# Kernel optimization log

Measured on AMD Instinct MI355X. Metric: run time of the kernel, lower is better.

## Reference

```python
import jax, jax.numpy as jnp
import numpy as np

N_NODES = 50000
N_EDGES = 800000
D_FEAT = 128
N_LAYERS = 3
HALF = 64  # units // 2 per kernel in tf_geometric MeanGraphSage
HIDDEN = 256
NUM_LABELS = 40


def setup_inputs() -> dict:
    key = jax.random.key(0)
    ks = jax.random.split(key, 6)
    x = jax.random.normal(ks[0], (N_NODES, D_FEAT), dtype=jnp.float32)
    edge_index = jax.random.randint(ks[1], (2, N_EDGES), 0, N_NODES, dtype=jnp.int32)
    self_kernels = jax.random.normal(ks[2], (N_LAYERS, D_FEAT, HALF), dtype=jnp.float32) * 0.05
    neighbor_kernels = jax.random.normal(ks[3], (N_LAYERS, D_FEAT, HALF), dtype=jnp.float32) * 0.05
    biases = jnp.zeros((N_LAYERS, 2 * HALF), dtype=jnp.float32)
    mlp_w1 = jax.random.normal(ks[4], (2 * HALF, HIDDEN), dtype=jnp.float32) * 0.05
    mlp_b1 = jnp.zeros((HIDDEN,), dtype=jnp.float32)
    mlp_w2 = jax.random.normal(ks[5], (HIDDEN, NUM_LABELS), dtype=jnp.float32) * 0.05
    mlp_b2 = jnp.zeros((NUM_LABELS,), dtype=jnp.float32)
    return {"x": x, "edge_index": edge_index, "self_kernels": self_kernels,
            "neighbor_kernels": neighbor_kernels, "biases": biases,
            "mlp_w1": mlp_w1, "mlp_b1": mlp_b1, "mlp_w2": mlp_w2, "mlp_b2": mlp_b2}


def reference(x, edge_index, self_kernels, neighbor_kernels, biases,
              mlp_w1, mlp_b1, mlp_w2, mlp_b2):
    n = x.shape[0]
    row, col = edge_index[0], edge_index[1]  # row: target node, col: source node
    # in-degree counts (graph is fixed across layers)
    ones = jnp.ones((edge_index.shape[1],), dtype=x.dtype)
    deg = jax.ops.segment_sum(ones, row, num_segments=n)  # [N]
    inv_deg = (1.0 / jnp.maximum(deg, 1.0))[:, None]      # [N,1]

    h = x
    for i in range(N_LAYERS):
        # mean-neighbor aggregation: gather source feats, segment-sum to targets
        nbr_sum = jax.ops.segment_sum(h[col], row, num_segments=n)  # [N,D]
        nbr_mean = nbr_sum * inv_deg
        from_self = h @ self_kernels[i]        # [N,HALF]
        from_nbr = nbr_mean @ neighbor_kernels[i]  # [N,HALF]
        h = jax.nn.relu(jnp.concatenate([from_self, from_nbr], axis=1) + biases[i])

    # MLP head (Flatten on [N,128] is a no-op)
    h = jax.nn.relu(h @ mlp_w1 + mlp_b1)
    return h @ mlp_w2 + mlp_b2
```

## Files before the change

kernel.cpp:

```cpp
#include <hip/hip_runtime.h>
#include <hip/hip_bf16.h>
#include <cstdint>
#include <cstddef>

#define N_NODES 50000
#define N_PAD   50176
#define N_EDGES 800000
#define D_FEAT  128
#define HALF    64
#define HIDDEN  256
#define LABELS  40

#define NBUCK 196
#define BCAP  5632
#define EDGES_PER_BLK 4096

#define HID_STRIDE 264

typedef __attribute__((ext_vector_type(8))) short bf16x8;
typedef __attribute__((ext_vector_type(4))) float f32x4;

#define PK_SELF(L) ((size_t)(L) * 8192)
#define PK_NBR(L)  (24576 + (size_t)(L) * 8192)
#define PK_W1      49152
#define PK_W2      81920
#define PK_TOTAL   94208

__device__ inline uint16_t f2bf_bits(float f) {
    __hip_bfloat16 b = __float2bfloat16(f);
    uint16_t u; __builtin_memcpy(&u, &b, 2); return u;
}

__global__ __launch_bounds__(1024) void bucket_scatter_kernel(
        const int* __restrict__ row, const int* __restrict__ col,
        int* __restrict__ bucket_cursor, uint32_t* __restrict__ staged) {
    __shared__ int hist[NBUCK];
    __shared__ int hbase[NBUCK];
    int tid  = threadIdx.x;
    int e0   = blockIdx.x * EDGES_PER_BLK;
    int eend = e0 + EDGES_PER_BLK; if (eend > N_EDGES) eend = N_EDGES;

    for (int i = tid; i < NBUCK; i += 1024) hist[i] = 0;
    __syncthreads();

    int rr[4], cc[4]; int ne = 0;
    for (int e = e0 + tid; e < eend; e += 1024) {
        rr[ne] = row[e]; cc[ne] = col[e]; ne++;
    }
    for (int i = 0; i < ne; i++) atomicAdd(&hist[rr[i] >> 8], 1);
    __syncthreads();

    for (int i = tid; i < NBUCK; i += 1024) {
        hbase[i] = atomicAdd(&bucket_cursor[i], hist[i]);
        hist[i]  = 0;
    }
    __syncthreads();

    for (int i = 0; i < ne; i++) {
        int b   = rr[i] >> 8;
        int off = atomicAdd(&hist[b], 1);
        int pos = hbase[b] + off;
        if (pos < BCAP)
            staged[(size_t)b * BCAP + pos] =
                ((uint32_t)(rr[i] & 255) << 16) | (uint32_t)cc[i];
    }
}

__global__ __launch_bounds__(1024) void bucket_fill_kernel(
        const uint32_t* __restrict__ staged, const int* __restrict__ bucket_cursor,
        int* __restrict__ deg, int* __restrict__ rowstart,
        float* __restrict__ inv_deg, int* __restrict__ csr_col) {
    __shared__ int cnt[256];
    __shared__ int excl[256];
    __shared__ int wt[4];
    __shared__ int seg[BCAP];
    __shared__ int base_s;
    int b   = blockIdx.x;
    int tid = threadIdx.x;

    if (tid < 64) {
        int partial = 0;
        for (int i = tid; i < b; i += 64) partial += bucket_cursor[i];
#pragma unroll
        for (int off = 32; off > 0; off >>= 1)
            partial += __shfl_down(partial, off, 64);
        if (tid == 0) base_s = partial;
    }
    if (tid < 256) cnt[tid] = 0;
    __syncthreads();

    int total = bucket_cursor[b]; if (total > BCAP) total = BCAP;
    int gbase = base_s;
    const uint32_t* st = staged + (size_t)b * BCAP;

    for (int i = tid; i < total; i += 1024) atomicAdd(&cnt[st[i] >> 16], 1);
    __syncthreads();

    int lane = tid & 63, wid = tid >> 6;
    int v = 0, s = 0;
    if (tid < 256) {
        v = cnt[tid]; s = v;
#pragma unroll
        for (int off = 1; off < 64; off <<= 1) {
            int t = __shfl_up(s, off, 64);
            if (lane >= off) s += t;
        }
        if (lane == 63) wt[wid] = s;
    }
    __syncthreads();
    if (tid == 0) { int a = 0; for (int i = 0; i < 4; i++) { int t = wt[i]; wt[i] = a; a += t; } }
    __syncthreads();
    if (tid < 256) {
        int ex = s - v + wt[wid];
        excl[tid] = ex;
        int node = (b << 8) + tid;
        if (node < N_NODES) {
            deg[node]      = v;
            rowstart[node] = gbase + ex;
            inv_deg[node]  = 1.0f / fmaxf((float)v, 1.0f);
        }
    }
    __syncthreads();
    for (int i = tid; i < total; i += 1024) {
        uint32_t u = st[i];
        int p = atomicAdd(&excl[u >> 16], 1);
        seg[p] = (int)(u & 0xffffu);
    }
    __syncthreads();
    for (int i = tid; i < total; i += 1024) csr_col[gbase + i] = seg[i];
}

__global__ __launch_bounds__(256) void xcast_kernel(
        const float* __restrict__ x, __hip_bfloat16* __restrict__ xb) {
    size_t i = (size_t)(blockIdx.x * blockDim.x + threadIdx.x) * 4;
    if (i >= (size_t)N_NODES * D_FEAT) return;
    float4 v = *(const float4*)(x + i);
    uint2 p;
    p.x = (uint32_t)f2bf_bits(v.x) | ((uint32_t)f2bf_bits(v.y) << 16);
    p.y = (uint32_t)f2bf_bits(v.z) | ((uint32_t)f2bf_bits(v.w) << 16);
    *(uint2*)((uint16_t*)xb + i) = p;
}

__global__ __launch_bounds__(256) void pack_all_kernel(
        const float* __restrict__ selfk, const float* __restrict__ nbrk,
        const float* __restrict__ w1, const float* __restrict__ w2,
        __hip_bfloat16* __restrict__ wpack) {
    int m = blockIdx.y;
    const float* W; int K, Ncols, Npad; size_t dstoff;
    if (m < 3)      { W = selfk + (size_t)m*D_FEAT*HALF;      K=128; Ncols=64;  Npad=64;  dstoff = PK_SELF(m); }
    else if (m < 6) { W = nbrk  + (size_t)(m-3)*D_FEAT*HALF;  K=128; Ncols=64;  Npad=64;  dstoff = PK_NBR(m-3); }
    else if (m == 6){ W = w1;                                 K=128; Ncols=256; Npad=256; dstoff = PK_W1; }
    else            { W = w2;                                 K=256; Ncols=40;  Npad=48;  dstoff = PK_W2; }
    int ksteps = K / 32;
    int total  = ksteps * (Npad / 16) * 64;
    int t = blockIdx.x * blockDim.x + threadIdx.x;
    if (t >= total) return;
    int lane = t & 63;
    int rest = t >> 6;
    int ks   = rest % ksteps;
    int ns   = rest / ksteps;
    int colb = ns * 16 + (lane & 15);
    int kb   = ks * 32 + (lane >> 4) * 8;
    __hip_bfloat16* dst = wpack + dstoff + (size_t)t * 8;
#pragma unroll
    for (int j = 0; j < 8; j++) {
        float v = (colb < Ncols) ? W[(size_t)(kb + j) * Ncols + colb] : 0.f;
        dst[j] = __float2bfloat16(v);
    }
}

__global__ __launch_bounds__(256) void agg4_kernel(
        const __hip_bfloat16* __restrict__ h, const int* __restrict__ csr_col,
        const int* __restrict__ rowstart, const int* __restrict__ deg,
        const float* __restrict__ inv_deg, __hip_bfloat16* __restrict__ nbr) {
    int gid  = blockIdx.x * blockDim.x + threadIdx.x;
    int wnum = gid >> 6;
    int lane = threadIdx.x & 63;
    int sub  = lane >> 4;
    int sl   = lane & 15;
    int node = wnum * 4 + sub;
    int start = rowstart[node];
    int d     = deg[node];
    const uint32_t* hw = (const uint32_t*)h;
    float acc[8] = {};

#define ACC8(U)                                        \
    acc[0] += __uint_as_float((U).x << 16);            \
    acc[1] += __uint_as_float((U).x & 0xffff0000u);    \
    acc[2] += __uint_as_float((U).y << 16);            \
    acc[3] += __uint_as_float((U).y & 0xffff0000u);    \
    acc[4] += __uint_as_float((U).z << 16);            \
    acc[5] += __uint_as_float((U).z & 0xffff0000u);    \
    acc[6] += __uint_as_float((U).w << 16);            \
    acc[7] += __uint_as_float((U).w & 0xffff0000u);

    if (d > 0) {
        int last = start + d - 1;
        int s[8];
#pragma unroll
        for (int k = 0; k < 8; k++) s[k] = csr_col[min(start + k, last)];
        int j = 0;
        for (; j + 8 <= d; j += 8) {
            int p[8];
#pragma unroll
            for (int k = 0; k < 8; k++) p[k] = csr_col[min(start + j + 8 + k, last)];
            uint4 u0 = *(const uint4*)(hw + (size_t)s[0] * 64 + sl * 4);
            uint4 u1 = *(const uint4*)(hw + (size_t)s[1] * 64 + sl * 4);
            uint4 u2 = *(const uint4*)(hw + (size_t)s[2] * 64 + sl * 4);
            uint4 u3 = *(const uint4*)(hw + (size_t)s[3] * 64 + sl * 4);
            uint4 u4 = *(const uint4*)(hw + (size_t)s[4] * 64 + sl * 4);
            uint4 u5 = *(const uint4*)(hw + (size_t)s[5] * 64 + sl * 4);
            uint4 u6 = *(const uint4*)(hw + (size_t)s[6] * 64 + sl * 4);
            uint4 u7 = *(const uint4*)(hw + (size_t)s[7] * 64 + sl * 4);
            ACC8(u0); ACC8(u1); ACC8(u2); ACC8(u3);
            ACC8(u4); ACC8(u5); ACC8(u6); ACC8(u7);
#pragma unroll
            for (int k = 0; k < 8; k++) s[k] = p[k];
        }
        int r = d - j;
#pragma unroll
        for (int k = 0; k < 8; k++) {
            if (k < r) {
                uint4 u = *(const uint4*)(hw + (size_t)s[k] * 64 + sl * 4);
                ACC8(u);
            }
        }
    }
#undef ACC8

    float inv = inv_deg[node];
    uint4 p;
    p.x = (uint32_t)f2bf_bits(acc[0] * inv) | ((uint32_t)f2bf_bits(acc[1] * inv) << 16);
    p.y = (uint32_t)f2bf_bits(acc[2] * inv) | ((uint32_t)f2bf_bits(acc[3] * inv) << 16);
    p.z = (uint32_t)f2bf_bits(acc[4] * inv) | ((uint32_t)f2bf_bits(acc[5] * inv) << 16);
    p.w = (uint32_t)f2bf_bits(acc[6] * inv) | ((uint32_t)f2bf_bits(acc[7] * inv) << 16);
    *(uint4*)((uint32_t*)nbr + (size_t)node * 64 + sl * 4) = p;
}

__global__ __launch_bounds__(256, 2) void layer_fused_kernel(
        const __hip_bfloat16* __restrict__ h, const __hip_bfloat16* __restrict__ nbr,
        const __hip_bfloat16* __restrict__ wpack_self,
        const __hip_bfloat16* __restrict__ wpack_nbr,
        const float* __restrict__ bias, __hip_bfloat16* __restrict__ out) {
    int wave = threadIdx.x >> 6, lane = threadIdx.x & 63;
    int row0 = blockIdx.x * 128 + wave * 32;
    int lrow = lane & 15, lgrp = lane >> 4;
    const __hip_bfloat16* hr0 = h   + (size_t)(row0 + lrow) * D_FEAT + lgrp * 8;
    const __hip_bfloat16* hr1 = hr0 + (size_t)16 * D_FEAT;
    const __hip_bfloat16* nr0 = nbr + (size_t)(row0 + lrow) * D_FEAT + lgrp * 8;
    const __hip_bfloat16* nr1 = nr0 + (size_t)16 * D_FEAT;

    f32x4 accS[2][4] = {};
    f32x4 accN[2][4] = {};
#pragma unroll
    for (int ks = 0; ks < 4; ks++) {
        bf16x8 ah0 = *(const bf16x8*)(hr0 + ks * 32);
        bf16x8 ah1 = *(const bf16x8*)(hr1 + ks * 32);
        bf16x8 an0 = *(const bf16x8*)(nr0 + ks * 32);
        bf16x8 an1 = *(const bf16x8*)(nr1 + ks * 32);
#pragma unroll
        for (int ns = 0; ns < 4; ns++) {
            bf16x8 bs = *(const bf16x8*)(wpack_self + ((size_t)(ns * 4 + ks) * 64 + lane) * 8);
            accS[0][ns] = __builtin_amdgcn_mfma_f32_16x16x32_bf16(ah0, bs, accS[0][ns], 0, 0, 0);
            accS[1][ns] = __builtin_amdgcn_mfma_f32_16x16x32_bf16(ah1, bs, accS[1][ns], 0, 0, 0);
            bf16x8 bn = *(const bf16x8*)(wpack_nbr + ((size_t)(ns * 4 + ks) * 64 + lane) * 8);
            accN[0][ns] = __builtin_amdgcn_mfma_f32_16x16x32_bf16(an0, bn, accN[0][ns], 0, 0, 0);
            accN[1][ns] = __builtin_amdgcn_mfma_f32_16x16x32_bf16(an1, bn, accN[1][ns], 0, 0, 0);
        }
    }
#pragma unroll
    for (int t = 0; t < 2; t++) {
#pragma unroll
        for (int ns = 0; ns < 4; ns++) {
            int colS = ns * 16 + lrow;
            int colN = HALF + colS;
            float bvS = bias[colS];
            float bvN = bias[colN];
#pragma unroll
            for (int i = 0; i < 4; i++) {
                int r = row0 + t * 16 + lgrp * 4 + i;
                out[(size_t)r * D_FEAT + colS] =
                    __float2bfloat16(fmaxf(accS[t][ns][i] + bvS, 0.f));
                out[(size_t)r * D_FEAT + colN] =
                    __float2bfloat16(fmaxf(accN[t][ns][i] + bvN, 0.f));
            }
        }
    }
}

__global__ __launch_bounds__(256, 2) void mlp_fused_kernel(
        const __hip_bfloat16* __restrict__ h, const __hip_bfloat16* __restrict__ w1p,
        const float* __restrict__ b1, const __hip_bfloat16* __restrict__ w2p,
        const float* __restrict__ b2, float* __restrict__ out) {
    __shared__ __align__(16) uint16_t hid[128 * HID_STRIDE];
    int wave = threadIdx.x >> 6, lane = threadIdx.x & 63;
    int row0 = blockIdx.x * 128 + wave * 32;
    int lrow = lane & 15, lgrp = lane >> 4;

    {
        const __hip_bfloat16* ar0 = h + (size_t)(row0 + lrow) * D_FEAT + lgrp * 8;
        const __hip_bfloat16* ar1 = ar0 + (size_t)16 * D_FEAT;
        f32x4 acc[2][16] = {};
#pragma unroll 1
        for (int ks = 0; ks < 4; ks++) {
            bf16x8 a0 = *(const bf16x8*)(ar0 + ks * 32);
            bf16x8 a1 = *(const bf16x8*)(ar1 + ks * 32);
#pragma unroll
            for (int ns = 0; ns < 16; ns++) {
                bf16x8 bfr = *(const bf16x8*)(w1p + ((size_t)(ns * 4 + ks) * 64 + lane) * 8);
                acc[0][ns] = __builtin_amdgcn_mfma_f32_16x16x32_bf16(a0, bfr, acc[0][ns], 0, 0, 0);
                acc[1][ns] = __builtin_amdgcn_mfma_f32_16x16x32_bf16(a1, bfr, acc[1][ns], 0, 0, 0);
            }
        }
        int lbase = wave * 32;
#pragma unroll
        for (int t = 0; t < 2; t++) {
#pragma unroll
            for (int ns = 0; ns < 16; ns++) {
                int col = ns * 16 + lrow;
                float bv = b1[col];
#pragma unroll
                for (int i = 0; i < 4; i++) {
                    int lr = lbase + t * 16 + lgrp * 4 + i;
                    hid[lr * HID_STRIDE + col] =
                        f2bf_bits(fmaxf(acc[t][ns][i] + bv, 0.f));
                }
            }
        }
    }
    __syncthreads();

    const uint16_t* br0 = &hid[(wave * 32 + lrow) * HID_STRIDE + lgrp * 8];
    const uint16_t* br1 = br0 + 16 * HID_STRIDE;
    f32x4 acc2[2][3] = {};
#pragma unroll
    for (int ks = 0; ks < 8; ks++) {
        bf16x8 a0 = *(const bf16x8*)(br0 + ks * 32);
        bf16x8 a1 = *(const bf16x8*)(br1 + ks * 32);
#pragma unroll
        for (int ns = 0; ns < 3; ns++) {
            bf16x8 bfr = *(const bf16x8*)(w2p + ((size_t)(ns * 8 + ks) * 64 + lane) * 8);
            acc2[0][ns] = __builtin_amdgcn_mfma_f32_16x16x32_bf16(a0, bfr, acc2[0][ns], 0, 0, 0);
            acc2[1][ns] = __builtin_amdgcn_mfma_f32_16x16x32_bf16(a1, bfr, acc2[1][ns], 0, 0, 0);
        }
    }
#pragma unroll
    for (int t = 0; t < 2; t++) {
#pragma unroll
        for (int ns = 0; ns < 3; ns++) {
            int col = ns * 16 + lrow;
            if (col < LABELS) {
                float bv = b2[col];
#pragma unroll
                for (int i = 0; i < 4; i++) {
                    int r = row0 + t * 16 + lgrp * 4 + i;
                    if (r < N_NODES)
                        out[(size_t)r * LABELS + col] = acc2[t][ns][i] + bv;
                }
            }
        }
    }
}

extern "C" void kernel_launch(void* const* d_in, const int* in_sizes, int n_in,
                              void* d_out, int out_size, void* d_ws, size_t ws_size,
                              hipStream_t stream) {
    const float* x      = (const float*)d_in[0];
    const int*   ei     = (const int*)d_in[1];
    const float* selfk  = (const float*)d_in[2];
    const float* nbrk   = (const float*)d_in[3];
    const float* biases = (const float*)d_in[4];
    const float* w1     = (const float*)d_in[5];
    const float* b1     = (const float*)d_in[6];
    const float* w2     = (const float*)d_in[7];
    const float* b2     = (const float*)d_in[8];
    float* out = (float*)d_out;

    const int* row = ei;
    const int* col = ei + N_EDGES;

    char* ws = (char*)d_ws;
    size_t off = 0;
    auto alloc = [&](size_t bytes) -> char* {
        char* p = ws + off;
        off = (off + bytes + 255) & ~(size_t)255;
        return p;
    };
    int*   deg       = (int*)  alloc((size_t)N_NODES * 4);
    int*   rowstart  = (int*)  alloc((size_t)N_NODES * 4);
    float* inv_deg   = (float*)alloc((size_t)N_NODES * 4);
    int*   bucket_cursor = (int*)alloc(256 * 4);
    int*   csr_col   = (int*)  alloc((size_t)N_EDGES * 4);
    uint32_t* staged = (uint32_t*)alloc((size_t)NBUCK * BCAP * 4);
    __hip_bfloat16* wpack  = (__hip_bfloat16*)alloc(PK_TOTAL * 2);
    __hip_bfloat16* xb     = (__hip_bfloat16*)alloc((size_t)N_PAD * D_FEAT * 2);
    __hip_bfloat16* hA     = (__hip_bfloat16*)alloc((size_t)N_PAD * D_FEAT * 2);
    __hip_bfloat16* hB     = (__hip_bfloat16*)alloc((size_t)N_PAD * D_FEAT * 2);
    __hip_bfloat16* nbrbuf = (__hip_bfloat16*)alloc((size_t)N_PAD * D_FEAT * 2);

    hipMemsetAsync(bucket_cursor, 0, 256 * 4, stream);

    const int scat_blocks = (N_EDGES + EDGES_PER_BLK - 1) / EDGES_PER_BLK;
    bucket_scatter_kernel<<<scat_blocks, 1024, 0, stream>>>(row, col, bucket_cursor, staged);
    bucket_fill_kernel<<<NBUCK, 1024, 0, stream>>>(staged, bucket_cursor,
                                                   deg, rowstart, inv_deg, csr_col);

    xcast_kernel<<<(N_NODES * D_FEAT / 4 + 255) / 256, 256, 0, stream>>>(x, xb);
    dim3 pgrid(16, 8);
    pack_all_kernel<<<pgrid, 256, 0, stream>>>(selfk, nbrk, w1, w2, wpack);

    const int agg_blocks   = N_NODES / 16;
    const int layer_blocks = N_PAD / 128;
    const int mlp_blocks   = N_PAD / 128;

    const __hip_bfloat16* hcur = xb;
    __hip_bfloat16* bufs[3] = {hA, hB, hA};
    for (int L = 0; L < 3; L++) {
        agg4_kernel<<<agg_blocks, 256, 0, stream>>>(hcur, csr_col, rowstart, deg,
                                                    inv_deg, nbrbuf);
        layer_fused_kernel<<<layer_blocks, 256, 0, stream>>>(
            hcur, nbrbuf, wpack + PK_SELF(L), wpack + PK_NBR(L),
            biases + (size_t)L * (2 * HALF), bufs[L]);
        hcur = bufs[L];
    }

    mlp_fused_kernel<<<mlp_blocks, 256, 0, stream>>>(hcur, wpack + PK_W1, b1,
                                                     wpack + PK_W2, b2, out);
}
```

Measured before the change: 247.6 us.

## Transform-then-aggregate: gather 64-wide fp16 projected neighbors instead of raw features

Reorders each layer so the neighbor projection (h @ W_nbr) runs before aggregation, because mean aggregation is linear. The gather then reads 64-wide fp16 rows instead of 128-wide bf16 rows, which halves the bytes read per edge in the dominant irregular gather. Bias, ReLU and the 1/deg scaling move into the aggregation kernel, which writes the upper half of h in place. The first GEMM reads fp32 x directly, removing the separate cast kernel. The intermediate is rounded to fp16, which adds overflow and precision risk.

```diff
diff --git a/kernel.cpp b/kernel.cpp
--- a/kernel.cpp
+++ b/kernel.cpp
@@ -1,5 +1,6 @@
 #include <hip/hip_runtime.h>
 #include <hip/hip_bf16.h>
+#include <hip/hip_fp16.h>
 #include <cstdint>
 #include <cstddef>
 
@@ -29,6 +30,11 @@
 __device__ inline uint16_t f2bf_bits(float f) {
     __hip_bfloat16 b = __float2bfloat16(f);
     uint16_t u; __builtin_memcpy(&u, &b, 2); return u;
+}
+
+__device__ inline float2 h2f(uint32_t u) {
+    __half2 h; __builtin_memcpy(&h, &u, 4);
+    return __half22float2(h);
 }
 
 __global__ __launch_bounds__(1024) void bucket_scatter_kernel(
@@ -128,17 +134,6 @@
     }
     __syncthreads();
     for (int i = tid; i < total; i += 1024) csr_col[gbase + i] = seg[i];
-}
-
-__global__ __launch_bounds__(256) void xcast_kernel(
-        const float* __restrict__ x, __hip_bfloat16* __restrict__ xb) {
-    size_t i = (size_t)(blockIdx.x * blockDim.x + threadIdx.x) * 4;
-    if (i >= (size_t)N_NODES * D_FEAT) return;
-    float4 v = *(const float4*)(x + i);
-    uint2 p;
-    p.x = (uint32_t)f2bf_bits(v.x) | ((uint32_t)f2bf_bits(v.y) << 16);
-    p.y = (uint32_t)f2bf_bits(v.z) | ((uint32_t)f2bf_bits(v.w) << 16);
-    *(uint2*)((uint16_t*)xb + i) = p;
 }
 
 __global__ __launch_bounds__(256) void pack_all_kernel(
@@ -169,30 +164,107 @@
     }
 }
 
-__global__ __launch_bounds__(256) void agg4_kernel(
-        const __hip_bfloat16* __restrict__ h, const int* __restrict__ csr_col,
+template<bool AF32>
+__global__ __launch_bounds__(256, 2) void layer_gemm_kernel(
+        const void* __restrict__ Ain,
+        const __hip_bfloat16* __restrict__ wpack_self,
+        const __hip_bfloat16* __restrict__ wpack_nbr,
+        const float* __restrict__ bias,
+        __hip_bfloat16* __restrict__ hout,
+        uint16_t* __restrict__ zn) {
+    int wave = threadIdx.x >> 6, lane = threadIdx.x & 63;
+    int row0 = blockIdx.x * 128 + wave * 32;
+    int lrow = lane & 15, lgrp = lane >> 4;
+
+    const __hip_bfloat16 *hr0 = nullptr, *hr1 = nullptr;
+    const float *xr0 = nullptr, *xr1 = nullptr;
+    if constexpr (AF32) {
+        const float* x = (const float*)Ain;
+        int r0 = min(row0 + lrow, N_NODES - 1);
+        int r1 = min(row0 + lrow + 16, N_NODES - 1);
+        xr0 = x + (size_t)r0 * D_FEAT + lgrp * 8;
+        xr1 = x + (size_t)r1 * D_FEAT + lgrp * 8;
+    } else {
+        const __hip_bfloat16* h = (const __hip_bfloat16*)Ain;
+        hr0 = h + (size_t)(row0 + lrow) * D_FEAT + lgrp * 8;
+        hr1 = hr0 + (size_t)16 * D_FEAT;
+    }
+
+    f32x4 accS[2][4] = {};
+    f32x4 accN[2][4] = {};
+#pragma unroll
+    for (int ks = 0; ks < 4; ks++) {
+        bf16x8 a0, a1;
+        if constexpr (AF32) {
+            float4 u0  = *(const float4*)(xr0 + ks * 32);
+            float4 u0b = *(const float4*)(xr0 + ks * 32 + 4);
+            float4 u1  = *(const float4*)(xr1 + ks * 32);
+            float4 u1b = *(const float4*)(xr1 + ks * 32 + 4);
+            float f0[8] = {u0.x, u0.y, u0.z, u0.w, u0b.x, u0b.y, u0b.z, u0b.w};
+            float f1[8] = {u1.x, u1.y, u1.z, u1.w, u1b.x, u1b.y, u1b.z, u1b.w};
+#pragma unroll
+            for (int j = 0; j < 8; j++) { a0[j] = (short)f2bf_bits(f0[j]); a1[j] = (short)f2bf_bits(f1[j]); }
+        } else {
+            a0 = *(const bf16x8*)(hr0 + ks * 32);
+            a1 = *(const bf16x8*)(hr1 + ks * 32);
+        }
+#pragma unroll
+        for (int ns = 0; ns < 4; ns++) {
+            bf16x8 bs = *(const bf16x8*)(wpack_self + ((size_t)(ns * 4 + ks) * 64 + lane) * 8);
+            accS[0][ns] = __builtin_amdgcn_mfma_f32_16x16x32_bf16(a0, bs, accS[0][ns], 0, 0, 0);
+            accS[1][ns] = __builtin_amdgcn_mfma_f32_16x16x32_bf16(a1, bs, accS[1][ns], 0, 0, 0);
+            bf16x8 bn = *(const bf16x8*)(wpack_nbr + ((size_t)(ns * 4 + ks) * 64 + lane) * 8);
+            accN[0][ns] = __builtin_amdgcn_mfma_f32_16x16x32_bf16(a0, bn, accN[0][ns], 0, 0, 0);
+            accN[1][ns] = __builtin_amdgcn_mfma_f32_16x16x32_bf16(a1, bn, accN[1][ns], 0, 0, 0);
+        }
+    }
+#pragma unroll
+    for (int t = 0; t < 2; t++) {
+#pragma unroll
+        for (int ns = 0; ns < 4; ns++) {
+            int colS = ns * 16 + lrow;
+            float bvS = bias[colS];
+#pragma unroll
+            for (int i = 0; i < 4; i++) {
+                int r = row0 + t * 16 + lgrp * 4 + i;
+                hout[(size_t)r * D_FEAT + colS] =
+                    __float2bfloat16(fmaxf(accS[t][ns][i] + bvS, 0.f));
+                __half hz = __float2half(accN[t][ns][i]);
+                uint16_t hb; __builtin_memcpy(&hb, &hz, 2);
+                zn[(size_t)r * HALF + colS] = hb;
+            }
+        }
+    }
+}
+
+__global__ __launch_bounds__(128) void agg8_kernel(
+        const uint16_t* __restrict__ zn, const int* __restrict__ csr_col,
         const int* __restrict__ rowstart, const int* __restrict__ deg,
-        const float* __restrict__ inv_deg, __hip_bfloat16* __restrict__ nbr) {
-    int gid  = blockIdx.x * blockDim.x + threadIdx.x;
+        const float* __restrict__ inv_deg, const float* __restrict__ bias64,
+        __hip_bfloat16* __restrict__ hout) {
+    int gid  = blockIdx.x * 128 + threadIdx.x;
     int wnum = gid >> 6;
     int lane = threadIdx.x & 63;
-    int sub  = lane >> 4;
-    int sl   = lane & 15;
-    int node = wnum * 4 + sub;
+    int sub  = lane >> 3;
+    int sl   = lane & 7;
+    int node = wnum * 8 + sub;
     int start = rowstart[node];
     int d     = deg[node];
-    const uint32_t* hw = (const uint32_t*)h;
+    const uint32_t* zw = (const uint32_t*)zn;
     float acc[8] = {};
 
-#define ACC8(U)                                        \
-    acc[0] += __uint_as_float((U).x << 16);            \
-    acc[1] += __uint_as_float((U).x & 0xffff0000u);    \
-    acc[2] += __uint_as_float((U).y << 16);            \
-    acc[3] += __uint_as_float((U).y & 0xffff0000u);    \
-    acc[4] += __uint_as_float((U).z << 16);            \
-    acc[5] += __uint_as_float((U).z & 0xffff0000u);    \
-    acc[6] += __uint_as_float((U).w << 16);            \
-    acc[7] += __uint_as_float((U).w & 0xffff0000u);
+#define ACC8H(U) { float2 t0 = h2f((U).x), t1 = h2f((U).y),            \
+                   float2_dummy_##__LINE__; (void)0;                    \
+    acc[0] += t0.x; acc[1] += t0.y; acc[2] += t1.x; acc[3] += t1.y;     \
+    float2 t2 = h2f((U).z), t3 = h2f((U).w);                            \
+    acc[4] += t2.x; acc[5] += t2.y; acc[6] += t3.x; acc[7] += t3.y; }
+
+#undef ACC8H
+#define ACC8H(U) {                                                      \
+    float2 t0 = h2f((U).x); acc[0] += t0.x; acc[1] += t0.y;             \
+    float2 t1 = h2f((U).y); acc[2] += t1.x; acc[3] += t1.y;             \
+    float2 t2 = h2f((U).z); acc[4] += t2.x; acc[5] += t2.y;             \
+    float2 t3 = h2f((U).w); acc[6] += t3.x; acc[7] += t3.y; }
 
     if (d > 0) {
         int last = start + d - 1;
@@ -204,16 +276,16 @@
             int p[8];
 #pragma unroll
             for (int k = 0; k < 8; k++) p[k] = csr_col[min(start + j + 8 + k, last)];
-            uint4 u0 = *(const uint4*)(hw + (size_t)s[0] * 64 + sl * 4);
-            uint4 u1 = *(const uint4*)(hw + (size_t)s[1] * 64 + sl * 4);
-            uint4 u2 = *(const uint4*)(hw + (size_t)s[2] * 64 + sl * 4);
-            uint4 u3 = *(const uint4*)(hw + (size_t)s[3] * 64 + sl * 4);
-            uint4 u4 = *(const uint4*)(hw + (size_t)s[4] * 64 + sl * 4);
-            uint4 u5 = *(const uint4*)(hw + (size_t)s[5] * 64 + sl * 4);
-            uint4 u6 = *(const uint4*)(hw + (size_t)s[6] * 64 + sl * 4);
-            uint4 u7 = *(const uint4*)(hw + (size_t)s[7] * 64 + sl * 4);
-            ACC8(u0); ACC8(u1); ACC8(u2); ACC8(u3);
-            ACC8(u4); ACC8(u5); ACC8(u6); ACC8(u7);
+            uint4 u0 = *(const uint4*)(zw + (size_t)s[0] * 32 + sl * 4);
+            uint4 u1 = *(const uint4*)(zw + (size_t)s[1] * 32 + sl * 4);
+            uint4 u2 = *(const uint4*)(zw + (size_t)s[2] * 32 + sl * 4);
+            uint4 u3 = *(const uint4*)(zw + (size_t)s[3] * 32 + sl * 4);
+            uint4 u4 = *(const uint4*)(zw + (size_t)s[4] * 32 + sl * 4);
+            uint4 u5 = *(const uint4*)(zw + (size_t)s[5] * 32 + sl * 4);
+            uint4 u6 = *(const uint4*)(zw + (size_t)s[6] * 32 + sl * 4);
+            uint4 u7 = *(const uint4*)(zw + (size_t)s[7] * 32 + sl * 4);
+            ACC8H(u0); ACC8H(u1); ACC8H(u2); ACC8H(u3);
+            ACC8H(u4); ACC8H(u5); ACC8H(u6); ACC8H(u7);
 #pragma unroll
             for (int k = 0; k < 8; k++) s[k] = p[k];
         }
@@ -221,71 +293,26 @@
 #pragma unroll
         for (int k = 0; k < 8; k++) {
             if (k < r) {
-                uint4 u = *(const uint4*)(hw + (size_t)s[k] * 64 + sl * 4);
-                ACC8(u);
+                uint4 u = *(const uint4*)(zw + (size_t)s[k] * 32 + sl * 4);
+                ACC8H(u);
             }
         }
     }
-#undef ACC8
+#undef ACC8H
 
     float inv = inv_deg[node];
+    float4 b0 = *(const float4*)(bias64 + sl * 8);
+    float4 b1 = *(const float4*)(bias64 + sl * 8 + 4);
     uint4 p;
-    p.x = (uint32_t)f2bf_bits(acc[0] * inv) | ((uint32_t)f2bf_bits(acc[1] * inv) << 16);
-    p.y = (uint32_t)f2bf_bits(acc[2] * inv) | ((uint32_t)f2bf_bits(acc[3] * inv) << 16);
-    p.z = (uint32_t)f2bf_bits(acc[4] * inv) | ((uint32_t)f2bf_bits(acc[5] * inv) << 16);
-    p.w = (uint32_t)f2bf_bits(acc[6] * inv) | ((uint32_t)f2bf_bits(acc[7] * inv) << 16);
-    *(uint4*)((uint32_t*)nbr + (size_t)node * 64 + sl * 4) = p;
-}
-
-__global__ __launch_bounds__(256, 2) void layer_fused_kernel(
-        const __hip_bfloat16* __restrict__ h, const __hip_bfloat16* __restrict__ nbr,
-        const __hip_bfloat16* __restrict__ wpack_self,
-        const __hip_bfloat16* __restrict__ wpack_nbr,
-        const float* __restrict__ bias, __hip_bfloat16* __restrict__ out) {
-    int wave = threadIdx.x >> 6, lane = threadIdx.x & 63;
-    int row0 = blockIdx.x * 128 + wave * 32;
-    int lrow = lane & 15, lgrp = lane >> 4;
-    const __hip_bfloat16* hr0 = h   + (size_t)(row0 + lrow) * D_FEAT + lgrp * 8;
-    const __hip_bfloat16* hr1 = hr0 + (size_t)16 * D_FEAT;
-    const __hip_bfloat16* nr0 = nbr + (size_t)(row0 + lrow) * D_FEAT + lgrp * 8;
-    const __hip_bfloat16* nr1 = nr0 + (size_t)16 * D_FEAT;
-
-    f32x4 accS[2][4] = {};
-    f32x4 accN[2][4] = {};
-#pragma unroll
-    for (int ks = 0; ks < 4; ks++) {
-        bf16x8 ah0 = *(const bf16x8*)(hr0 + ks * 32);
-        bf16x8 ah1 = *(const bf16x8*)(hr1 + ks * 32);
-        bf16x8 an0 = *(const bf16x8*)(nr0 + ks * 32);
-        bf16x8 an1 = *(const bf16x8*)(nr1 + ks * 32);
-#pragma unroll
-        for (int ns = 0; ns < 4; ns++) {
-            bf16x8 bs = *(const bf16x8*)(wpack_self + ((size_t)(ns * 4 + ks) * 64 + lane) * 8);
-            accS[0][ns] = __builtin_amdgcn_mfma_f32_16x16x32_bf16(ah0, bs, accS[0][ns], 0, 0, 0);
-            accS[1][ns] = __builtin_amdgcn_mfma_f32_16x16x32_bf16(ah1, bs, accS[1][ns], 0, 0, 0);
-            bf16x8 bn = *(const bf16x8*)(wpack_nbr + ((size_t)(ns * 4 + ks) * 64 + lane) * 8);
-            accN[0][ns] = __builtin_amdgcn_mfma_f32_16x16x32_bf16(an0, bn, accN[0][ns], 0, 0, 0);
-            accN[1][ns] = __builtin_amdgcn_mfma_f32_16x16x32_bf16(an1, bn, accN[1][ns], 0, 0, 0);
-        }
-    }
-#pragma unroll
-    for (int t = 0; t < 2; t++) {
-#pragma unroll
-        for (int ns = 0; ns < 4; ns++) {
-            int colS = ns * 16 + lrow;
-            int colN = HALF + colS;
-            float bvS = bias[colS];
-            float bvN = bias[colN];
-#pragma unroll
-            for (int i = 0; i < 4; i++) {
-                int r = row0 + t * 16 + lgrp * 4 + i;
-                out[(size_t)r * D_FEAT + colS] =
-                    __float2bfloat16(fmaxf(accS[t][ns][i] + bvS, 0.f));
-                out[(size_t)r * D_FEAT + colN] =
-                    __float2bfloat16(fmaxf(accN[t][ns][i] + bvN, 0.f));
-            }
-        }
-    }
+    p.x = (uint32_t)f2bf_bits(fmaxf(acc[0] * inv + b0.x, 0.f))
+        | ((uint32_t)f2bf_bits(fmaxf(acc[1] * inv + b0.y, 0.f)) << 16);
+    p.y = (uint32_t)f2bf_bits(fmaxf(acc[2] * inv + b0.z, 0.f))
+        | ((uint32_t)f2bf_bits(fmaxf(acc[3] * inv + b0.w, 0.f)) << 16);
+    p.z = (uint32_t)f2bf_bits(fmaxf(acc[4] * inv + b1.x, 0.f))
+        | ((uint32_t)f2bf_bits(fmaxf(acc[5] * inv + b1.y, 0.f)) << 16);
+    p.w = (uint32_t)f2bf_bits(fmaxf(acc[6] * inv + b1.z, 0.f))
+        | ((uint32_t)f2bf_bits(fmaxf(acc[7] * inv + b1.w, 0.f)) << 16);
+    *(uint4*)((uint32_t*)hout + (size_t)node * 64 + 32 + sl * 4) = p;
 }
 
 __global__ __launch_bounds__(256, 2) void mlp_fused_kernel(
@@ -393,10 +420,9 @@
     int*   csr_col   = (int*)  alloc((size_t)N_EDGES * 4);
     uint32_t* staged = (uint32_t*)alloc((size_t)NBUCK * BCAP * 4);
     __hip_bfloat16* wpack  = (__hip_bfloat16*)alloc(PK_TOTAL * 2);
-    __hip_bfloat16* xb     = (__hip_bfloat16*)alloc((size_t)N_PAD * D_FEAT * 2);
     __hip_bfloat16* hA     = (__hip_bfloat16*)alloc((size_t)N_PAD * D_FEAT * 2);
     __hip_bfloat16* hB     = (__hip_bfloat16*)alloc((size_t)N_PAD * D_FEAT * 2);
-    __hip_bfloat16* nbrbuf = (__hip_bfloat16*)alloc((size_t)N_PAD * D_FEAT * 2);
+    uint16_t*       zn     = (uint16_t*)alloc((size_t)N_PAD * HALF * 2);
 
     hipMemsetAsync(bucket_cursor, 0, 256 * 4, stream);
 
@@ -405,25 +431,25 @@
     bucket_fill_kernel<<<NBUCK, 1024, 0, stream>>>(staged, bucket_cursor,
                                                    deg, rowstart, inv_deg, csr_col);
 
-    xcast_kernel<<<(N_NODES * D_FEAT / 4 + 255) / 256, 256, 0, stream>>>(x, xb);
     dim3 pgrid(16, 8);
     pack_all_kernel<<<pgrid, 256, 0, stream>>>(selfk, nbrk, w1, w2, wpack);
 
+    const int layer_blocks = N_PAD / 128;
     const int agg_blocks   = N_NODES / 16;
-    const int layer_blocks = N_PAD / 128;
-    const int mlp_blocks   = N_PAD / 128;
-
-    const __hip_bfloat16* hcur = xb;
-    __hip_bfloat16* bufs[3] = {hA, hB, hA};
-    for (int L = 0; L < 3; L++) {
-        agg4_kernel<<<agg_blocks, 256, 0, stream>>>(hcur, csr_col, rowstart, deg,
-                                                    inv_deg, nbrbuf);
-        layer_fused_kernel<<<layer_blocks, 256, 0, stream>>>(
-            hcur, nbrbuf, wpack + PK_SELF(L), wpack + PK_NBR(L),
-            biases + (size_t)L * (2 * HALF), bufs[L]);
-        hcur = bufs[L];
-    }
-
-    mlp_fused_kernel<<<mlp_blocks, 256, 0, stream>>>(hcur, wpack + PK_W1, b1,
-                                                     wpack + PK_W2, b2, out);
-}
+
+    layer_gemm_kernel<true><<<layer_blocks, 256, 0, stream>>>(
+        (const void*)x, wpack + PK_SELF(0), wpack + PK_NBR(0), biases, hA, zn);
+    agg8_kernel<<<agg_blocks, 128, 0, stream>>>(zn, csr_col, rowstart, deg,
+                                                inv_deg, biases + 64, hA);
+    layer_gemm_kernel<false><<<layer_blocks, 256, 0, stream>>>(
+        (const void*)hA, wpack + PK_SELF(1), wpack + PK_NBR(1), biases + 128, hB, zn);
+    agg8_kernel<<<agg_blocks, 128, 0, stream>>>(zn, csr_col, rowstart, deg,
+                                                inv_deg, biases + 128 + 64, hB);
+    layer_gemm_kernel<false><<<layer_blocks, 256, 0, stream>>>(
+        (const void*)hB, wpack + PK_SELF(2), wpack + PK_NBR(2), biases + 256, hA, zn);
+    agg8_kernel<<<agg_blocks, 128, 0, stream>>>(zn, csr_col, rowstart, deg,
+                                                inv_deg, biases + 256 + 64, hA);
+
+    mlp_fused_kernel<<<layer_blocks, 256, 0, stream>>>(hA, wpack + PK_W1, b1,
+                                                       wpack + PK_W2, b2, out);
+}
```

Result: faster. 206.3 us (-16.7%).
